# Performance work log

Hardware: AMD Instinct MI355X
Metric: run time of the kernel (lower is better)

Reference implementation:

```python
import jax, jax.numpy as jnp
import numpy as np

T, B, D, E, H = 64, 1024, 128, 256, 512


def _gru(x_emb, h0, W_ih, W_hh, b_ih, b_hh):
    """Standard GRU (PyTorch gate convention) over time-major x_emb [T,B,E]."""
    xW = x_emb @ W_ih + b_ih  # [T,B,3H], precompute input contractions

    def step(h, xw):
        hW = h @ W_hh + b_hh
        xr, xz, xn = jnp.split(xw, 3, axis=-1)
        hr, hz, hn = jnp.split(hW, 3, axis=-1)
        r = jax.nn.sigmoid(xr + hr)
        z = jax.nn.sigmoid(xz + hz)
        n = jnp.tanh(xn + r * hn)
        h_new = (1.0 - z) * n + z * h
        return h_new, h_new

    h_t, ys = jax.lax.scan(step, h0, xW)
    return ys, h_t


def setup_inputs() -> dict:
    key = jax.random.key(0)
    ks = jax.random.split(key, 16)
    s_in = 1.0 / np.sqrt(D)
    s_emb = 1.0 / np.sqrt(E)
    s_hid = 1.0 / np.sqrt(H)
    return {
        "past_input": jax.random.normal(ks[0], (T, B, D), jnp.float32),
        "future_input": jax.random.normal(ks[1], (T, B, D), jnp.float32),
        "noise": jax.random.normal(ks[2], (B, H), jnp.float32),
        "W_emb": jax.random.normal(ks[3], (D, E), jnp.float32) * s_in,
        "b_emb": jnp.zeros((E,), jnp.float32),
        "W_ih_enc": jax.random.normal(ks[4], (E, 3 * H), jnp.float32) * s_emb,
        "W_hh_enc": jax.random.normal(ks[5], (H, 3 * H), jnp.float32) * s_hid,
        "b_ih_enc": jnp.zeros((3 * H,), jnp.float32),
        "b_hh_enc": jnp.zeros((3 * H,), jnp.float32),
        "W_ih_dec": jax.random.normal(ks[6], (E, 3 * H), jnp.float32) * s_emb,
        "W_hh_dec": jax.random.normal(ks[7], (H, 3 * H), jnp.float32) * s_hid,
        "b_ih_dec": jnp.zeros((3 * H,), jnp.float32),
        "b_hh_dec": jnp.zeros((3 * H,), jnp.float32),
        "W_out": jax.random.normal(ks[8], (H, D), jnp.float32) * s_hid,
        "b_out": jnp.zeros((D,), jnp.float32),
    }


def reference(past_input, future_input, noise, W_emb, b_emb,
              W_ih_enc, W_hh_enc, b_ih_enc, b_hh_enc,
              W_ih_dec, W_hh_dec, b_ih_dec, b_hh_dec,
              W_out, b_out):
    past_emb = jax.nn.relu(past_input @ W_emb + b_emb)      # [T,B,E]
    fut_emb = jax.nn.relu(future_input @ W_emb + b_emb)     # [T,B,E]

    h0 = jnp.zeros((past_emb.shape[1], W_hh_enc.shape[0]), past_emb.dtype)
    _, h_t = _gru(past_emb, h0, W_ih_enc, W_hh_enc, b_ih_enc, b_hh_enc)

    # shift future embedding: step 0 -> zeros, step t -> emb at t-1
    fut_shift = jnp.concatenate([jnp.zeros_like(fut_emb[:1]), fut_emb[:-1]], axis=0)

    hidden = h_t + noise
    future_target, _ = _gru(fut_shift, hidden, W_ih_dec, W_hh_dec, b_ih_dec, b_hh_dec)
    return future_target @ W_out + b_out  # [T,B,D]
```

## Files before the change

kernel.cpp:

```cpp
#include <hip/hip_runtime.h>

typedef __bf16 bf16;
typedef __bf16 bf16x8 __attribute__((ext_vector_type(8)));
typedef float f32x4 __attribute__((ext_vector_type(4)));

#define Tt 64
#define Bb 1024
#define Dd 128
#define Ee 256
#define Hh 512
#define H3 1536

__device__ __forceinline__ float sigmf(float x) { return 1.0f / (1.0f + __expf(-x)); }
__device__ __forceinline__ float tanhfast(float x) {
    float e = __expf(2.0f * x);
    return 1.0f - 2.0f / (e + 1.0f);
}

#define LD_SC(dst, bp, OFF) \
    asm volatile("global_load_dwordx4 %0, %1, off offset:" #OFF " sc1" : "=&v"(dst) : "v"(bp))
#define ST_SC(bp, OFF, val) \
    asm volatile("global_store_short %0, %1, off offset:" #OFF " sc1" :: "v"(bp), "v"(val))

__global__ void k_prep(const float* __restrict__ We, const float* __restrict__ Wie, const float* __restrict__ Whe,
                       const float* __restrict__ Wid, const float* __restrict__ Whd, const float* __restrict__ Wo,
                       bf16* __restrict__ dWe, bf16* __restrict__ dWie, bf16* __restrict__ dWhe,
                       bf16* __restrict__ dWid, bf16* __restrict__ dWhd, bf16* __restrict__ dWo) {
    long i = (long)blockIdx.x * 256 + threadIdx.x;
    const float* s;
    bf16* d;
    int K, N;
    if (i < 32768) { s = We; d = dWe; K = Dd; N = Ee; }
    else if ((i -= 32768) < 393216) { s = Wie; d = dWie; K = Ee; N = H3; }
    else if ((i -= 393216) < 786432) { s = Whe; d = dWhe; K = Hh; N = H3; }
    else if ((i -= 786432) < 393216) { s = Wid; d = dWid; K = Ee; N = H3; }
    else if ((i -= 393216) < 786432) { s = Whd; d = dWhd; K = Hh; N = H3; }
    else if ((i -= 786432) < 65536) { s = Wo; d = dWo; K = Hh; N = Dd; }
    else return;
    int n = (int)(i / K), k = (int)(i - (long)n * K);
    d[i] = (bf16)s[(size_t)k * N + n];
}

__global__ __launch_bounds__(256) void k_embed(const float* __restrict__ xP, const float* __restrict__ xF,
                                               const bf16* __restrict__ WT, const float* __restrict__ bias,
                                               bf16* __restrict__ oP, bf16* __restrict__ oF) {
    const int lane = threadIdx.x & 63, wv = threadIdx.x >> 6;
    const float* x = blockIdx.z ? xF : xP;
    bf16* o = blockIdx.z ? oF : oP;
    const int m0w = blockIdx.x * 128 + wv * 32;
    const int c0 = blockIdx.y * 64;
    const int koff = (lane >> 4) * 8;
    f32x4 acc[2][4];
#pragma unroll
    for (int m = 0; m < 2; ++m)
#pragma unroll
        for (int s = 0; s < 4; ++s) acc[m][s] = f32x4{0.f, 0.f, 0.f, 0.f};

    const float* xp0 = x + (size_t)(m0w + (lane & 15)) * Dd + koff;
#pragma unroll
    for (int kc = 0; kc < 4; ++kc) {
        bf16x8 a0, a1;
        {
            float4 f0 = *(const float4*)(xp0 + kc * 32);
            float4 f1 = *(const float4*)(xp0 + kc * 32 + 4);
            a0[0] = (bf16)f0.x; a0[1] = (bf16)f0.y; a0[2] = (bf16)f0.z; a0[3] = (bf16)f0.w;
            a0[4] = (bf16)f1.x; a0[5] = (bf16)f1.y; a0[6] = (bf16)f1.z; a0[7] = (bf16)f1.w;
            float4 g0 = *(const float4*)(xp0 + 16 * Dd + kc * 32);
            float4 g1 = *(const float4*)(xp0 + 16 * Dd + kc * 32 + 4);
            a1[0] = (bf16)g0.x; a1[1] = (bf16)g0.y; a1[2] = (bf16)g0.z; a1[3] = (bf16)g0.w;
            a1[4] = (bf16)g1.x; a1[5] = (bf16)g1.y; a1[6] = (bf16)g1.z; a1[7] = (bf16)g1.w;
        }
#pragma unroll
        for (int s = 0; s < 4; ++s) {
            bf16x8 b = *(const bf16x8*)(WT + (size_t)(c0 + s * 16 + (lane & 15)) * Dd + kc * 32 + koff);
            acc[0][s] = __builtin_amdgcn_mfma_f32_16x16x32_bf16(a0, b, acc[0][s], 0, 0, 0);
            acc[1][s] = __builtin_amdgcn_mfma_f32_16x16x32_bf16(a1, b, acc[1][s], 0, 0, 0);
        }
    }
#pragma unroll
    for (int m = 0; m < 2; ++m)
#pragma unroll
        for (int s = 0; s < 4; ++s) {
            int col = c0 + s * 16 + (lane & 15);
            float bv = bias[col];
#pragma unroll
            for (int r = 0; r < 4; ++r) {
                int row = m0w + m * 16 + (lane >> 4) * 4 + r;
                o[(size_t)row * Ee + col] = (bf16)fmaxf(acc[m][s][r] + bv, 0.0f);
            }
        }
}

__global__ __launch_bounds__(256, 1) void k_gru_all(
    const bf16* __restrict__ embP, const bf16* __restrict__ embF, const float* __restrict__ noise,
    const bf16* __restrict__ WihE, const bf16* __restrict__ WhhE,
    const float* __restrict__ bIhE, const float* __restrict__ bHhE,
    const bf16* __restrict__ WihD, const bf16* __restrict__ WhhD,
    const float* __restrict__ bIhD, const float* __restrict__ bHhD,
    bf16* __restrict__ hA, bf16* __restrict__ hB, bf16* __restrict__ ys, unsigned* __restrict__ flags) {
    __shared__ bf16 Wih[6 * 8 * 64 * 8];
    __shared__ bf16 Whh[6 * 16 * 64 * 8];
    const int tid = threadIdx.x;
    const int lane = tid & 63, rh = tid >> 6;
    const int bid = blockIdx.x;
    const int im = (bid & 7) * 2 + (bid >> 7);
    const int in = (bid >> 3) & 15;
    const int rowb = im * 64 + rh * 16;
    const int arow0 = rowb + (lane & 15);
    const int koff = (lane >> 4) * 8;
    const int colc0 = in * 32 + (lane & 15);
    unsigned* dom = flags + ((size_t)im * 4 + rh) * 16 * 16;

    const bf16x8* WihV = (const bf16x8*)Wih;
    const bf16x8* WhhV = (const bf16x8*)Whh;

    auto stage = [&](const bf16* WT, int Kdim, int KC, bf16* lds) {
        int total = 6 * KC * 64;
        for (int idx = tid; idx < total; idx += 256) {
            int ln = idx & 63;
            int kc = (idx >> 6) % KC;
            int s = (idx >> 6) / KC;
            int gate = s >> 1, f = s & 1;
            int col = gate * Hh + in * 32 + f * 16 + (ln & 15);
            int k = kc * 32 + (ln >> 4) * 8;
            *(bf16x8*)(lds + (size_t)idx * 8) = *(const bf16x8*)(WT + (size_t)col * Kdim + k);
        }
    };

    float bi[3][2], bh[3][2];
    auto load_bias = [&](const float* bIh, const float* bHh) {
#pragma unroll
        for (int g = 0; g < 3; ++g)
#pragma unroll
            for (int f = 0; f < 2; ++f) {
                int c = g * Hh + colc0 + f * 16;
                bi[g][f] = bIh[c];
                bh[g][f] = bHh[c];
            }
    };

    auto signal = [&](unsigned seq) {
        asm volatile("s_waitcnt vmcnt(0)" ::: "memory");
        if (lane == 0) {
            unsigned* fp = dom + in * 16;
            asm volatile("global_store_dword %0, %1, off sc1" :: "v"(fp), "v"(seq) : "memory");
        }
    };
    auto poll = [&](unsigned seq) -> unsigned long long {
        unsigned v;
        const unsigned* fp = dom + (lane & 15) * 16;
        asm volatile("global_load_dword %0, %1, off sc1\n\ts_waitcnt vmcnt(0)"
                     : "=&v"(v) : "v"(fp) : "memory");
        return __ballot((int)(v >= seq));
    };
    auto wait_all = [&](unsigned seq) {
        while (poll(seq) != ~0ULL) __builtin_amdgcn_s_sleep(2);
    };

    f32x4 aR[2], aZ[2], aNX[2], aNH[2];
    auto zacc = [&]() {
#pragma unroll
        for (int f = 0; f < 2; ++f) {
            aR[f] = f32x4{0.f, 0.f, 0.f, 0.f};
            aZ[f] = f32x4{0.f, 0.f, 0.f, 0.f};
            aNX[f] = f32x4{0.f, 0.f, 0.f, 0.f};
            aNH[f] = f32x4{0.f, 0.f, 0.f, 0.f};
        }
    };

    auto xp_phase = [&](const bf16* xp) {
        const bf16* ap = xp + (size_t)arow0 * Ee + koff;
#pragma unroll
        for (int kc = 0; kc < 8; ++kc) {
            bf16x8 a = *(const bf16x8*)(ap + kc * 32);
#pragma unroll
            for (int f = 0; f < 2; ++f) {
                aR[f] = __builtin_amdgcn_mfma_f32_16x16x32_bf16(a, WihV[((0 + f) * 8 + kc) * 64 + lane], aR[f], 0, 0, 0);
                aZ[f] = __builtin_amdgcn_mfma_f32_16x16x32_bf16(a, WihV[((2 + f) * 8 + kc) * 64 + lane], aZ[f], 0, 0, 0);
                aNX[f] = __builtin_amdgcn_mfma_f32_16x16x32_bf16(a, WihV[((4 + f) * 8 + kc) * 64 + lane], aNX[f], 0, 0, 0);
            }
        }
    };

    auto hw_phase = [&](const bf16* hp, unsigned seq) {
        const bf16* h0p = hp + (size_t)arow0 * Hh + koff;
        bf16x8 h0[16];
        unsigned long long rdy = poll(seq);
#define HSTEP(p, OFF) \
        while (!((rdy >> p) & 1ULL)) { __builtin_amdgcn_s_sleep(2); rdy = poll(seq); } \
        LD_SC(h0[p], h0p, OFF);
        HSTEP(0, 0)    HSTEP(1, 64)   HSTEP(2, 128)  HSTEP(3, 192)
        HSTEP(4, 256)  HSTEP(5, 320)  HSTEP(6, 384)  HSTEP(7, 448)
        HSTEP(8, 512)  HSTEP(9, 576)  HSTEP(10, 640) HSTEP(11, 704)
        HSTEP(12, 768) HSTEP(13, 832) HSTEP(14, 896) HSTEP(15, 960)
#undef HSTEP
        asm volatile("s_waitcnt vmcnt(0)" ::: "memory");
        __builtin_amdgcn_sched_barrier(0);
#pragma unroll
        for (int kc = 0; kc < 16; ++kc) {
#pragma unroll
            for (int f = 0; f < 2; ++f) {
                aR[f] = __builtin_amdgcn_mfma_f32_16x16x32_bf16(h0[kc], WhhV[((0 + f) * 16 + kc) * 64 + lane], aR[f], 0, 0, 0);
                aZ[f] = __builtin_amdgcn_mfma_f32_16x16x32_bf16(h0[kc], WhhV[((2 + f) * 16 + kc) * 64 + lane], aZ[f], 0, 0, 0);
                aNH[f] = __builtin_amdgcn_mfma_f32_16x16x32_bf16(h0[kc], WhhV[((4 + f) * 16 + kc) * 64 + lane], aNH[f], 0, 0, 0);
            }
        }
    };

    float hreg[8];
#pragma unroll
    for (int i = 0; i < 8; ++i) hreg[i] = 0.0f;

    auto epi = [&](bf16* op) {
#pragma unroll
        for (int f = 0; f < 2; ++f) {
            bf16* stb = op + (size_t)(rowb + (lane >> 4) * 4) * Hh + colc0 + f * 16;
            unsigned short us[4];
#pragma unroll
            for (int r = 0; r < 4; ++r) {
                float rg = sigmf(aR[f][r] + bi[0][f] + bh[0][f]);
                float zg = sigmf(aZ[f][r] + bi[1][f] + bh[1][f]);
                float ng = tanhfast(aNX[f][r] + bi[2][f] + rg * (aNH[f][r] + bh[2][f]));
                float hv = (1.0f - zg) * ng + zg * hreg[f * 4 + r];
                hreg[f * 4 + r] = hv;
                us[r] = __builtin_bit_cast(unsigned short, (bf16)hv);
            }
            ST_SC(stb, 0, us[0]);
            ST_SC(stb, 1024, us[1]);
            ST_SC(stb, 2048, us[2]);
            ST_SC(stb, 3072, us[3]);
        }
    };

    stage(WihE, Ee, 8, Wih);
    stage(WhhE, Hh, 16, Whh);
    load_bias(bIhE, bHhE);
    __syncthreads();

#pragma unroll 1
    for (int t = 0; t < Tt; ++t) {
        zacc();
        xp_phase(embP + (size_t)t * Bb * Ee);
        if (t > 0) hw_phase(((t - 1) & 1) ? hB : hA, (unsigned)t);
        epi((t & 1) ? hB : hA);
        signal((unsigned)(t + 1));
    }

    wait_all((unsigned)Tt);
    {
#pragma unroll
        for (int f = 0; f < 2; ++f) {
            bf16* stb = hA + (size_t)(rowb + (lane >> 4) * 4) * Hh + colc0 + f * 16;
            unsigned short us[4];
#pragma unroll
            for (int r = 0; r < 4; ++r) {
                int row = rowb + (lane >> 4) * 4 + r;
                float v = hreg[f * 4 + r] + noise[(size_t)row * Hh + colc0 + f * 16];
                hreg[f * 4 + r] = v;
                us[r] = __builtin_bit_cast(unsigned short, (bf16)v);
            }
            ST_SC(stb, 0, us[0]);
            ST_SC(stb, 1024, us[1]);
            ST_SC(stb, 2048, us[2]);
            ST_SC(stb, 3072, us[3]);
        }
    }
    __syncthreads();
    stage(WihD, Ee, 8, Wih);
    stage(WhhD, Hh, 16, Whh);
    __syncthreads();
    load_bias(bIhD, bHhD);
    signal((unsigned)(Tt + 1));

#pragma unroll 1
    for (int t = 0; t < Tt; ++t) {
        zacc();
        if (t > 0) xp_phase(embF + (size_t)(t - 1) * Bb * Ee);
        hw_phase(t ? ys + (size_t)(t - 1) * Bb * Hh : hA, (unsigned)(Tt + 1 + t));
        epi(ys + (size_t)t * Bb * Hh);
        if (t < Tt - 1) signal((unsigned)(Tt + 2 + t));
    }
}

__global__ __launch_bounds__(256) void k_out(const bf16* __restrict__ ys, const bf16* __restrict__ WT,
                                             const float* __restrict__ bias, float* __restrict__ out) {
    const int lane = threadIdx.x & 63, wv = threadIdx.x >> 6;
    const int m0w = blockIdx.x * 256 + wv * 64;
    const int c0 = blockIdx.y * 64;
    const int koff = (lane >> 4) * 8;
    f32x4 acc[4][4];
#pragma unroll
    for (int m = 0; m < 4; ++m)
#pragma unroll
        for (int s = 0; s < 4; ++s) acc[m][s] = f32x4{0.f, 0.f, 0.f, 0.f};

    const bf16* ap = ys + (size_t)(m0w + (lane & 15)) * Hh + koff;
#pragma unroll
    for (int kc = 0; kc < 16; ++kc) {
        bf16x8 a0 = *(const bf16x8*)(ap + kc * 32);
        bf16x8 a1 = *(const bf16x8*)(ap + 16 * Hh + kc * 32);
        bf16x8 a2 = *(const bf16x8*)(ap + 32 * Hh + kc * 32);
        bf16x8 a3 = *(const bf16x8*)(ap + 48 * Hh + kc * 32);
#pragma unroll
        for (int s = 0; s < 4; ++s) {
            bf16x8 b = *(const bf16x8*)(WT + (size_t)(c0 + s * 16 + (lane & 15)) * Hh + kc * 32 + koff);
            acc[0][s] = __builtin_amdgcn_mfma_f32_16x16x32_bf16(a0, b, acc[0][s], 0, 0, 0);
            acc[1][s] = __builtin_amdgcn_mfma_f32_16x16x32_bf16(a1, b, acc[1][s], 0, 0, 0);
            acc[2][s] = __builtin_amdgcn_mfma_f32_16x16x32_bf16(a2, b, acc[2][s], 0, 0, 0);
            acc[3][s] = __builtin_amdgcn_mfma_f32_16x16x32_bf16(a3, b, acc[3][s], 0, 0, 0);
        }
    }
#pragma unroll
    for (int m = 0; m < 4; ++m)
#pragma unroll
        for (int s = 0; s < 4; ++s) {
            int col = c0 + s * 16 + (lane & 15);
            float bv = bias[col];
#pragma unroll
            for (int r = 0; r < 4; ++r) {
                int row = m0w + m * 16 + (lane >> 4) * 4 + r;
                out[(size_t)row * Dd + col] = acc[m][s][r] + bv;
            }
        }
}

extern "C" void kernel_launch(void* const* d_in, const int* in_sizes, int n_in,
                              void* d_out, int out_size, void* d_ws, size_t ws_size,
                              hipStream_t stream) {
    const float* past = (const float*)d_in[0];
    const float* fut = (const float*)d_in[1];
    const float* noise = (const float*)d_in[2];
    const float* W_emb = (const float*)d_in[3];
    const float* b_emb = (const float*)d_in[4];
    const float* W_ih_enc = (const float*)d_in[5];
    const float* W_hh_enc = (const float*)d_in[6];
    const float* b_ih_enc = (const float*)d_in[7];
    const float* b_hh_enc = (const float*)d_in[8];
    const float* W_ih_dec = (const float*)d_in[9];
    const float* W_hh_dec = (const float*)d_in[10];
    const float* b_ih_dec = (const float*)d_in[11];
    const float* b_hh_dec = (const float*)d_in[12];
    const float* W_out = (const float*)d_in[13];
    const float* b_out = (const float*)d_in[14];
    float* out = (float*)d_out;

    char* w = (char*)d_ws;
    auto alloc = [&](size_t bytes) {
        char* p = w;
        w += (bytes + 255) & ~(size_t)255;
        return p;
    };
    bf16* embP = (bf16*)alloc((size_t)Tt * Bb * Ee * 2);
    bf16* embF = (bf16*)alloc((size_t)Tt * Bb * Ee * 2);
    bf16* ys = (bf16*)alloc((size_t)Tt * Bb * Hh * 2);
    bf16* hA = (bf16*)alloc((size_t)Bb * Hh * 2);
    bf16* hB = (bf16*)alloc((size_t)Bb * Hh * 2);
    bf16* WembT = (bf16*)alloc((size_t)Ee * Dd * 2);
    bf16* WihEncT = (bf16*)alloc((size_t)H3 * Ee * 2);
    bf16* WhhEncT = (bf16*)alloc((size_t)H3 * Hh * 2);
    bf16* WihDecT = (bf16*)alloc((size_t)H3 * Ee * 2);
    bf16* WhhDecT = (bf16*)alloc((size_t)H3 * Hh * 2);
    bf16* WoutT = (bf16*)alloc((size_t)Dd * Hh * 2);
    unsigned* flags = (unsigned*)alloc(16 * 4 * 16 * 16 * sizeof(unsigned));

    k_prep<<<9600, 256, 0, stream>>>(W_emb, W_ih_enc, W_hh_enc, W_ih_dec, W_hh_dec, W_out,
                                     WembT, WihEncT, WhhEncT, WihDecT, WhhDecT, WoutT);

    k_embed<<<dim3(Tt * Bb / 128, Ee / 64, 2), 256, 0, stream>>>(past, fut, WembT, b_emb, embP, embF);

    hipMemsetAsync(flags, 0, 16 * 4 * 16 * 16 * sizeof(unsigned), stream);

    void* args[] = {(void*)&embP, (void*)&embF, (void*)&noise,
                    (void*)&WihEncT, (void*)&WhhEncT, (void*)&b_ih_enc, (void*)&b_hh_enc,
                    (void*)&WihDecT, (void*)&WhhDecT, (void*)&b_ih_dec, (void*)&b_hh_dec,
                    (void*)&hA, (void*)&hB, (void*)&ys, (void*)&flags};
    hipLaunchCooperativeKernel((const void*)k_gru_all, dim3(256), dim3(256), args, 0, stream);

    k_out<<<dim3(Tt * Bb / 256, Dd / 64), 256, 0, stream>>>(ys, WoutT, b_out, out);
}
```

Before: 1.004 ms.

## Replace flag-based inter-block sync with sentinel-value polling on hidden state data

Removes the per-step flag signal/poll protocol between blocks. Each block now loads the previous hidden state directly and retries any chunk that still holds the 0xFFFF bf16 sentinel (a NaN pattern pre-filled by memset). To avoid reuse hazards, the encoder writes every timestep into its own buffer instead of ping-ponging two buffers. This cuts the signal store, the vmcnt wait and the flag round-trip from the critical path of the recurrence. In exchange it adds large memsets of ys and henc each call, and it relies on the GRU never producing the sentinel bit pattern.

```diff
diff --git a/kernel.cpp b/kernel.cpp
--- a/kernel.cpp
+++ b/kernel.cpp
@@ -3,6 +3,7 @@
 typedef __bf16 bf16;
 typedef __bf16 bf16x8 __attribute__((ext_vector_type(8)));
 typedef float f32x4 __attribute__((ext_vector_type(4)));
+typedef unsigned uint32x4 __attribute__((ext_vector_type(4)));
 
 #define Tt 64
 #define Bb 1024
@@ -21,6 +22,16 @@
     asm volatile("global_load_dwordx4 %0, %1, off offset:" #OFF " sc1" : "=&v"(dst) : "v"(bp))
 #define ST_SC(bp, OFF, val) \
     asm volatile("global_store_short %0, %1, off offset:" #OFF " sc1" :: "v"(bp), "v"(val))
+
+__device__ __forceinline__ bool has_sent(bf16x8 v) {
+    uint32x4 w = __builtin_bit_cast(uint32x4, v);
+    bool m = false;
+#pragma unroll
+    for (int i = 0; i < 4; ++i) {
+        m = m || ((w[i] & 0xFFFFu) == 0xFFFFu) || ((w[i] >> 16) == 0xFFFFu);
+    }
+    return m;
+}
 
 __global__ void k_prep(const float* __restrict__ We, const float* __restrict__ Wie, const float* __restrict__ Whe,
                        const float* __restrict__ Wid, const float* __restrict__ Whd, const float* __restrict__ Wo,
@@ -97,7 +108,7 @@
     const float* __restrict__ bIhE, const float* __restrict__ bHhE,
     const bf16* __restrict__ WihD, const bf16* __restrict__ WhhD,
     const float* __restrict__ bIhD, const float* __restrict__ bHhD,
-    bf16* __restrict__ hA, bf16* __restrict__ hB, bf16* __restrict__ ys, unsigned* __restrict__ flags) {
+    bf16* __restrict__ henc, bf16* __restrict__ hmid, bf16* __restrict__ ys) {
     __shared__ bf16 Wih[6 * 8 * 64 * 8];
     __shared__ bf16 Whh[6 * 16 * 64 * 8];
     const int tid = threadIdx.x;
@@ -109,7 +120,6 @@
     const int arow0 = rowb + (lane & 15);
     const int koff = (lane >> 4) * 8;
     const int colc0 = in * 32 + (lane & 15);
-    unsigned* dom = flags + ((size_t)im * 4 + rh) * 16 * 16;
 
     const bf16x8* WihV = (const bf16x8*)Wih;
     const bf16x8* WhhV = (const bf16x8*)Whh;
@@ -139,24 +149,6 @@
             }
     };
 
-    auto signal = [&](unsigned seq) {
-        asm volatile("s_waitcnt vmcnt(0)" ::: "memory");
-        if (lane == 0) {
-            unsigned* fp = dom + in * 16;
-            asm volatile("global_store_dword %0, %1, off sc1" :: "v"(fp), "v"(seq) : "memory");
-        }
-    };
-    auto poll = [&](unsigned seq) -> unsigned long long {
-        unsigned v;
-        const unsigned* fp = dom + (lane & 15) * 16;
-        asm volatile("global_load_dword %0, %1, off sc1\n\ts_waitcnt vmcnt(0)"
-                     : "=&v"(v) : "v"(fp) : "memory");
-        return __ballot((int)(v >= seq));
-    };
-    auto wait_all = [&](unsigned seq) {
-        while (poll(seq) != ~0ULL) __builtin_amdgcn_s_sleep(2);
-    };
-
     f32x4 aR[2], aZ[2], aNX[2], aNH[2];
     auto zacc = [&]() {
 #pragma unroll
@@ -182,19 +174,36 @@
         }
     };
 
-    auto hw_phase = [&](const bf16* hp, unsigned seq) {
+    auto hw_phase = [&](const bf16* hp) {
         const bf16* h0p = hp + (size_t)arow0 * Hh + koff;
         bf16x8 h0[16];
-        unsigned long long rdy = poll(seq);
-#define HSTEP(p, OFF) \
-        while (!((rdy >> p) & 1ULL)) { __builtin_amdgcn_s_sleep(2); rdy = poll(seq); } \
-        LD_SC(h0[p], h0p, OFF);
-        HSTEP(0, 0)    HSTEP(1, 64)   HSTEP(2, 128)  HSTEP(3, 192)
-        HSTEP(4, 256)  HSTEP(5, 320)  HSTEP(6, 384)  HSTEP(7, 448)
-        HSTEP(8, 512)  HSTEP(9, 576)  HSTEP(10, 640) HSTEP(11, 704)
-        HSTEP(12, 768) HSTEP(13, 832) HSTEP(14, 896) HSTEP(15, 960)
-#undef HSTEP
+        LD_SC(h0[0], h0p, 0);    LD_SC(h0[1], h0p, 64);   LD_SC(h0[2], h0p, 128);  LD_SC(h0[3], h0p, 192);
+        LD_SC(h0[4], h0p, 256);  LD_SC(h0[5], h0p, 320);  LD_SC(h0[6], h0p, 384);  LD_SC(h0[7], h0p, 448);
+        LD_SC(h0[8], h0p, 512);  LD_SC(h0[9], h0p, 576);  LD_SC(h0[10], h0p, 640); LD_SC(h0[11], h0p, 704);
+        LD_SC(h0[12], h0p, 768); LD_SC(h0[13], h0p, 832); LD_SC(h0[14], h0p, 896); LD_SC(h0[15], h0p, 960);
         asm volatile("s_waitcnt vmcnt(0)" ::: "memory");
+        unsigned fail = 0;
+#define CK0(p) fail |= ((unsigned)__any((int)has_sent(h0[p]))) << p;
+        CK0(0) CK0(1) CK0(2) CK0(3) CK0(4) CK0(5) CK0(6) CK0(7)
+        CK0(8) CK0(9) CK0(10) CK0(11) CK0(12) CK0(13) CK0(14) CK0(15)
+#undef CK0
+#pragma unroll 1
+        while (fail) {
+            __builtin_amdgcn_s_sleep(1);
+#define RT(p, OFF) if (fail & (1u << p)) { LD_SC(h0[p], h0p, OFF); }
+            RT(0, 0)    RT(1, 64)   RT(2, 128)  RT(3, 192)
+            RT(4, 256)  RT(5, 320)  RT(6, 384)  RT(7, 448)
+            RT(8, 512)  RT(9, 576)  RT(10, 640) RT(11, 704)
+            RT(12, 768) RT(13, 832) RT(14, 896) RT(15, 960)
+#undef RT
+            asm volatile("s_waitcnt vmcnt(0)" ::: "memory");
+            unsigned nf = 0;
+#define CK(p) if (fail & (1u << p)) { nf |= ((unsigned)__any((int)has_sent(h0[p]))) << p; }
+            CK(0) CK(1) CK(2) CK(3) CK(4) CK(5) CK(6) CK(7)
+            CK(8) CK(9) CK(10) CK(11) CK(12) CK(13) CK(14) CK(15)
+#undef CK
+            fail = nf;
+        }
         __builtin_amdgcn_sched_barrier(0);
 #pragma unroll
         for (int kc = 0; kc < 16; ++kc) {
@@ -241,16 +250,14 @@
     for (int t = 0; t < Tt; ++t) {
         zacc();
         xp_phase(embP + (size_t)t * Bb * Ee);
-        if (t > 0) hw_phase(((t - 1) & 1) ? hB : hA, (unsigned)t);
-        epi((t & 1) ? hB : hA);
-        signal((unsigned)(t + 1));
-    }
-
-    wait_all((unsigned)Tt);
+        if (t > 0) hw_phase(henc + (size_t)(t - 1) * Bb * Hh);
+        epi(henc + (size_t)t * Bb * Hh);
+    }
+
     {
 #pragma unroll
         for (int f = 0; f < 2; ++f) {
-            bf16* stb = hA + (size_t)(rowb + (lane >> 4) * 4) * Hh + colc0 + f * 16;
+            bf16* stb = hmid + (size_t)(rowb + (lane >> 4) * 4) * Hh + colc0 + f * 16;
             unsigned short us[4];
 #pragma unroll
             for (int r = 0; r < 4; ++r) {
@@ -270,15 +277,13 @@
     stage(WhhD, Hh, 16, Whh);
     __syncthreads();
     load_bias(bIhD, bHhD);
-    signal((unsigned)(Tt + 1));
 
 #pragma unroll 1
     for (int t = 0; t < Tt; ++t) {
         zacc();
         if (t > 0) xp_phase(embF + (size_t)(t - 1) * Bb * Ee);
-        hw_phase(t ? ys + (size_t)(t - 1) * Bb * Hh : hA, (unsigned)(Tt + 1 + t));
+        hw_phase(t ? ys + (size_t)(t - 1) * Bb * Hh : hmid);
         epi(ys + (size_t)t * Bb * Hh);
-        if (t < Tt - 1) signal((unsigned)(Tt + 2 + t));
     }
 }
 
@@ -353,27 +358,28 @@
     bf16* embP = (bf16*)alloc((size_t)Tt * Bb * Ee * 2);
     bf16* embF = (bf16*)alloc((size_t)Tt * Bb * Ee * 2);
     bf16* ys = (bf16*)alloc((size_t)Tt * Bb * Hh * 2);
-    bf16* hA = (bf16*)alloc((size_t)Bb * Hh * 2);
-    bf16* hB = (bf16*)alloc((size_t)Bb * Hh * 2);
+    bf16* henc = (bf16*)alloc((size_t)Tt * Bb * Hh * 2);
+    bf16* hmid = (bf16*)alloc((size_t)Bb * Hh * 2);
     bf16* WembT = (bf16*)alloc((size_t)Ee * Dd * 2);
     bf16* WihEncT = (bf16*)alloc((size_t)H3 * Ee * 2);
     bf16* WhhEncT = (bf16*)alloc((size_t)H3 * Hh * 2);
     bf16* WihDecT = (bf16*)alloc((size_t)H3 * Ee * 2);
     bf16* WhhDecT = (bf16*)alloc((size_t)H3 * Hh * 2);
     bf16* WoutT = (bf16*)alloc((size_t)Dd * Hh * 2);
-    unsigned* flags = (unsigned*)alloc(16 * 4 * 16 * 16 * sizeof(unsigned));
 
     k_prep<<<9600, 256, 0, stream>>>(W_emb, W_ih_enc, W_hh_enc, W_ih_dec, W_hh_dec, W_out,
                                      WembT, WihEncT, WhhEncT, WihDecT, WhhDecT, WoutT);
 
     k_embed<<<dim3(Tt * Bb / 128, Ee / 64, 2), 256, 0, stream>>>(past, fut, WembT, b_emb, embP, embF);
 
-    hipMemsetAsync(flags, 0, 16 * 4 * 16 * 16 * sizeof(unsigned), stream);
+    hipMemsetAsync(ys, 0xFF, (size_t)Tt * Bb * Hh * 2, stream);
+    hipMemsetAsync(henc, 0xFF, (size_t)Tt * Bb * Hh * 2, stream);
+    hipMemsetAsync(hmid, 0xFF, (size_t)Bb * Hh * 2, stream);
 
     void* args[] = {(void*)&embP, (void*)&embF, (void*)&noise,
                     (void*)&WihEncT, (void*)&WhhEncT, (void*)&b_ih_enc, (void*)&b_hh_enc,
                     (void*)&WihDecT, (void*)&WhhDecT, (void*)&b_ih_dec, (void*)&b_hh_dec,
-                    (void*)&hA, (void*)&hB, (void*)&ys, (void*)&flags};
+                    (void*)&henc, (void*)&hmid, (void*)&ys};
     hipLaunchCooperativeKernel((const void*)k_gru_all, dim3(256), dim3(256), args, 0, stream);
 
     k_out<<<dim3(Tt * Bb / 256, Dd / 64), 256, 0, stream>>>(ys, WoutT, b_out, out);
```

After: 1.160 ms. 15.5% more time.

## Fuse output projection into decoder GRU steps using already-loaded hidden state

Applied to the files above, without the earlier changes.

Removes the separate k_out GEMM kernel and computes the output projection inside the cooperative GRU kernel. Each block with in<8 reuses the h(t-1) fragments it already loaded for the recurrent matmul and applies 16 extra MFMAs against W_out read straight from global memory. After the loop, those blocks run one extra hw_phase to project the final step. This saves a kernel launch and a re-read of ys, but it adds work and global loads to the serial critical path, spread unevenly so that half the blocks carry the extra cost at every step.

```diff
diff --git a/kernel.cpp b/kernel.cpp
--- a/kernel.cpp
+++ b/kernel.cpp
@@ -97,6 +97,7 @@
     const float* __restrict__ bIhE, const float* __restrict__ bHhE,
     const bf16* __restrict__ WihD, const bf16* __restrict__ WhhD,
     const float* __restrict__ bIhD, const float* __restrict__ bHhD,
+    const bf16* __restrict__ WoT, const float* __restrict__ b_out, float* __restrict__ out,
     bf16* __restrict__ hA, bf16* __restrict__ hB, bf16* __restrict__ ys, unsigned* __restrict__ flags) {
     __shared__ bf16 Wih[6 * 8 * 64 * 8];
     __shared__ bf16 Whh[6 * 16 * 64 * 8];
@@ -110,6 +111,10 @@
     const int koff = (lane >> 4) * 8;
     const int colc0 = in * 32 + (lane & 15);
     unsigned* dom = flags + ((size_t)im * 4 + rh) * 16 * 16;
+    const bool doOut = (in < 8);
+    const int ocol = in * 16 + (lane & 15);
+    const float bo = doOut ? b_out[ocol] : 0.0f;
+    const bf16* wob = WoT + (size_t)ocol * Hh + koff;
 
     const bf16x8* WihV = (const bf16x8*)Wih;
     const bf16x8* WhhV = (const bf16x8*)Whh;
@@ -182,7 +187,7 @@
         }
     };
 
-    auto hw_phase = [&](const bf16* hp, unsigned seq) {
+    auto hw_phase = [&](const bf16* hp, unsigned seq, float* outp) {
         const bf16* h0p = hp + (size_t)arow0 * Hh + koff;
         bf16x8 h0[16];
         unsigned long long rdy = poll(seq);
@@ -205,6 +210,17 @@
                 aNH[f] = __builtin_amdgcn_mfma_f32_16x16x32_bf16(h0[kc], WhhV[((4 + f) * 16 + kc) * 64 + lane], aNH[f], 0, 0, 0);
             }
         }
+        if (outp) {
+            f32x4 oacc = f32x4{0.f, 0.f, 0.f, 0.f};
+#pragma unroll
+            for (int kc = 0; kc < 16; ++kc) {
+                bf16x8 b = *(const bf16x8*)(wob + kc * 32);
+                oacc = __builtin_amdgcn_mfma_f32_16x16x32_bf16(h0[kc], b, oacc, 0, 0, 0);
+            }
+            float* op = outp + (size_t)(rowb + (lane >> 4) * 4) * Dd + ocol;
+#pragma unroll
+            for (int r = 0; r < 4; ++r) op[(size_t)r * Dd] = oacc[r] + bo;
+        }
     };
 
     float hreg[8];
@@ -241,7 +257,7 @@
     for (int t = 0; t < Tt; ++t) {
         zacc();
         xp_phase(embP + (size_t)t * Bb * Ee);
-        if (t > 0) hw_phase(((t - 1) & 1) ? hB : hA, (unsigned)t);
+        if (t > 0) hw_phase(((t - 1) & 1) ? hB : hA, (unsigned)t, nullptr);
         epi((t & 1) ? hB : hA);
         signal((unsigned)(t + 1));
     }
@@ -276,52 +292,15 @@
     for (int t = 0; t < Tt; ++t) {
         zacc();
         if (t > 0) xp_phase(embF + (size_t)(t - 1) * Bb * Ee);
-        hw_phase(t ? ys + (size_t)(t - 1) * Bb * Hh : hA, (unsigned)(Tt + 1 + t));
+        float* outp = (t > 0 && doOut) ? out + (size_t)(t - 1) * Bb * Dd : nullptr;
+        hw_phase(t ? ys + (size_t)(t - 1) * Bb * Hh : hA, (unsigned)(Tt + 1 + t), outp);
         epi(ys + (size_t)t * Bb * Hh);
-        if (t < Tt - 1) signal((unsigned)(Tt + 2 + t));
-    }
-}
-
-__global__ __launch_bounds__(256) void k_out(const bf16* __restrict__ ys, const bf16* __restrict__ WT,
-                                             const float* __restrict__ bias, float* __restrict__ out) {
-    const int lane = threadIdx.x & 63, wv = threadIdx.x >> 6;
-    const int m0w = blockIdx.x * 256 + wv * 64;
-    const int c0 = blockIdx.y * 64;
-    const int koff = (lane >> 4) * 8;
-    f32x4 acc[4][4];
-#pragma unroll
-    for (int m = 0; m < 4; ++m)
-#pragma unroll
-        for (int s = 0; s < 4; ++s) acc[m][s] = f32x4{0.f, 0.f, 0.f, 0.f};
-
-    const bf16* ap = ys + (size_t)(m0w + (lane & 15)) * Hh + koff;
-#pragma unroll
-    for (int kc = 0; kc < 16; ++kc) {
-        bf16x8 a0 = *(const bf16x8*)(ap + kc * 32);
-        bf16x8 a1 = *(const bf16x8*)(ap + 16 * Hh + kc * 32);
-        bf16x8 a2 = *(const bf16x8*)(ap + 32 * Hh + kc * 32);
-        bf16x8 a3 = *(const bf16x8*)(ap + 48 * Hh + kc * 32);
-#pragma unroll
-        for (int s = 0; s < 4; ++s) {
-            bf16x8 b = *(const bf16x8*)(WT + (size_t)(c0 + s * 16 + (lane & 15)) * Hh + kc * 32 + koff);
-            acc[0][s] = __builtin_amdgcn_mfma_f32_16x16x32_bf16(a0, b, acc[0][s], 0, 0, 0);
-            acc[1][s] = __builtin_amdgcn_mfma_f32_16x16x32_bf16(a1, b, acc[1][s], 0, 0, 0);
-            acc[2][s] = __builtin_amdgcn_mfma_f32_16x16x32_bf16(a2, b, acc[2][s], 0, 0, 0);
-            acc[3][s] = __builtin_amdgcn_mfma_f32_16x16x32_bf16(a3, b, acc[3][s], 0, 0, 0);
-        }
-    }
-#pragma unroll
-    for (int m = 0; m < 4; ++m)
-#pragma unroll
-        for (int s = 0; s < 4; ++s) {
-            int col = c0 + s * 16 + (lane & 15);
-            float bv = bias[col];
-#pragma unroll
-            for (int r = 0; r < 4; ++r) {
-                int row = m0w + m * 16 + (lane >> 4) * 4 + r;
-                out[(size_t)row * Dd + col] = acc[m][s][r] + bv;
-            }
-        }
+        signal((unsigned)(Tt + 2 + t));
+    }
+
+    if (doOut) {
+        hw_phase(ys + (size_t)(Tt - 1) * Bb * Hh, (unsigned)(2 * Tt + 1), out + (size_t)(Tt - 1) * Bb * Dd);
+    }
 }
 
 extern "C" void kernel_launch(void* const* d_in, const int* in_sizes, int n_in,
@@ -373,8 +352,7 @@
     void* args[] = {(void*)&embP, (void*)&embF, (void*)&noise,
                     (void*)&WihEncT, (void*)&WhhEncT, (void*)&b_ih_enc, (void*)&b_hh_enc,
                     (void*)&WihDecT, (void*)&WhhDecT, (void*)&b_ih_dec, (void*)&b_hh_dec,
+                    (void*)&WoutT, (void*)&b_out, (void*)&out,
                     (void*)&hA, (void*)&hB, (void*)&ys, (void*)&flags};
     hipLaunchCooperativeKernel((const void*)k_gru_all, dim3(256), dim3(256), args, 0, stream);
-
-    k_out<<<dim3(Tt * Bb / 256, Dd / 64), 256, 0, stream>>>(ys, WoutT, b_out, out);
-}
+}
```

Result: slower. 1.034 ms (+3.0%).
